# Performance work log

Hardware: AMD Instinct MI355X
Metric: run time of the kernel (lower is better)

The kernel has to match this reference:

```python
import jax, jax.numpy as jnp
import numpy as np

N, E, R, G, IN, H, C = 100000, 400000, 4, 64, 64, 128, 2


def setup_inputs() -> dict:
    key = jax.random.key(0)
    ks = jax.random.split(key, 20)
    s = 0.05
    inp = {
        "x": jax.random.normal(ks[0], (N, IN), jnp.float32),
        "src": jax.random.randint(ks[1], (R, E), 0, N, jnp.int32),
        "dst": jax.random.randint(ks[2], (R, E), 0, N, jnp.int32),
        "graph_ids": jnp.sort(jax.random.randint(ks[3], (N,), 0, G, jnp.int32)),
        "W_in": jax.random.normal(ks[4], (IN, H), jnp.float32) * s,
        "b_in": jnp.zeros((H,), jnp.float32),
        "W1": jax.random.normal(ks[5], (R, H, H), jnp.float32) * s,
        "b1": jnp.zeros((R, H), jnp.float32),
        "W2": jax.random.normal(ks[6], (R, H, H), jnp.float32) * s,
        "b2": jnp.zeros((R, H), jnp.float32),
        "Wm1": jax.random.normal(ks[7], (H, H), jnp.float32) * s,
        "bm1": jnp.zeros((H,), jnp.float32),
        "Wm2": jax.random.normal(ks[8], (H, H), jnp.float32) * s,
        "bm2": jnp.zeros((H,), jnp.float32),
        "Wm3": jax.random.normal(ks[9], (H, C), jnp.float32) * s,
        "bm3": jnp.zeros((C,), jnp.float32),
    }
    return inp


def _gconv(x, src, dst, W, b):
    # DGL GraphConv, norm='both': D_in^{-1/2} A^T D_out^{-1/2} x W + b
    ones_e = jnp.ones(src.shape[0], x.dtype)
    deg_out = jnp.maximum(jax.ops.segment_sum(ones_e, src, num_segments=N), 1.0)
    deg_in = jnp.maximum(jax.ops.segment_sum(ones_e, dst, num_segments=N), 1.0)
    m = x * jax.lax.rsqrt(deg_out)[:, None]          # [N,H] normalized source feats
    agg = jax.ops.segment_sum(m[src], dst, num_segments=N)  # scatter-add over edges
    agg = agg * jax.lax.rsqrt(deg_in)[:, None]
    return agg @ W + b


def _hetero_layer(x, src, dst, W, b):
    # HeteroGraphConv with aggregate='sum' over relations
    out = jnp.zeros((N, W.shape[-1]), x.dtype)
    for r in range(R):
        out = out + _gconv(x, src[r], dst[r], W[r], b[r])
    return out


def reference(x, src, dst, graph_ids, W_in, b_in, W1, b1, W2, b2, Wm1, bm1, Wm2, bm2, Wm3, bm3):
    h = jax.nn.relu(x @ W_in + b_in)                 # input_linear + ReLU
    h = jax.nn.relu(_hetero_layer(h, src, dst, W1, b1))  # RGCN conv1 + ReLU
    h = _hetero_layer(h, src, dst, W2, b2)               # RGCN conv2
    # per-graph mean pooling (replaces the Python element loop)
    counts = jnp.maximum(jax.ops.segment_sum(jnp.ones(N, h.dtype), graph_ids, num_segments=G), 1.0)
    pooled = jax.ops.segment_sum(h, graph_ids, num_segments=G) / counts[:, None]
    # MLP head
    z = jax.nn.relu(pooled @ Wm1 + bm1)
    z = jax.nn.relu(z @ Wm2 + bm2)
    return z @ Wm3 + bm3                             # [G, C]
```

## Files before the change

kernel.cpp:

```cpp
#include <hip/hip_runtime.h>

constexpr int kN = 100000;
constexpr int kE = 400000;
constexpr int kR = 4;
constexpr int kG = 64;
constexpr int kIN = 64;
constexpr int kH = 128;
constexpr int kC = 2;
constexpr int kMAXD = 24;

constexpr size_t SZ_HB16 = (size_t)kN * kH * 2;
constexpr size_t SZ_RN   = (size_t)kR * kN * 4;
constexpr size_t OFF_HA   = 0;
constexpr size_t OFF_HB   = OFF_HA + SZ_HB16;
constexpr size_t OFF_DEGO = OFF_HB + SZ_HB16;
constexpr size_t OFF_CNT  = OFF_DEGO + SZ_RN;
constexpr size_t OFF_RSO  = OFF_CNT + SZ_RN;
constexpr size_t OFF_ELL  = OFF_RSO + SZ_RN;
constexpr size_t OFF_POOL = OFF_ELL + (size_t)kR * kN * kMAXD * 8;
constexpr size_t OFF_Z1   = OFF_POOL + (size_t)kG * kH * 4;
constexpr size_t OFF_Z2   = OFF_Z1 + (size_t)kG * kH * 4;
constexpr size_t OFF_WB1  = OFF_Z2 + (size_t)kG * kH * 4;
constexpr size_t OFF_WB2  = OFF_WB1 + (size_t)kH * kR * kH * 2;

typedef __attribute__((ext_vector_type(8))) short bf16x8;
typedef __attribute__((ext_vector_type(4))) float f32x4;

__device__ inline unsigned short f2bf(float f) {
    unsigned u = __builtin_bit_cast(unsigned, f);
    u += 0x7FFFu + ((u >> 16) & 1u);
    return (unsigned short)(u >> 16);
}
__device__ inline float bf2f_lo(unsigned p) {
    unsigned u = p << 16;
    return __builtin_bit_cast(float, u);
}
__device__ inline float bf2f_hi(unsigned p) {
    unsigned u = p & 0xFFFF0000u;
    return __builtin_bit_cast(float, u);
}


__global__ void k_deg(const int* __restrict__ src, int* __restrict__ deg_o) {
    int i = blockIdx.x * blockDim.x + threadIdx.x;
    if (i >= kR * kE) return;
    int r = i / kE;
    atomicAdd(&deg_o[r * kN + src[i]], 1);
}

__global__ void k_rs(const int* __restrict__ deg, float* __restrict__ rs) {
    int i = blockIdx.x * blockDim.x + threadIdx.x;
    if (i >= kR * kN) return;
    rs[i] = rsqrtf((float)max(deg[i], 1));
}

__global__ void k_fill(const int* __restrict__ src, const int* __restrict__ dst,
                       const float* __restrict__ rs_o, int* __restrict__ cnt,
                       int2* __restrict__ ell) {
    int i = blockIdx.x * blockDim.x + threadIdx.x;
    if (i >= kR * kE) return;
    int r = i / kE;
    int s = src[i], d = dst[i];
    int pos = atomicAdd(&cnt[r * kN + d], 1);
    if (pos < kMAXD) {
        float co = rs_o[r * kN + s];
        ell[(size_t)(r * kN + d) * kMAXD + pos] = make_int2(s, __builtin_bit_cast(int, co));
    }
}

__global__ void k_wconv(const float* __restrict__ W, unsigned short* __restrict__ Wbt) {
    int i = blockIdx.x * 256 + threadIdx.x;
    if (i >= kR * kH * kH) return;
    int r = i >> 14; int kk = (i >> 7) & 127; int j = i & 127;
    Wbt[(size_t)j * (kR * kH) + r * kH + kk] = f2bf(W[i]);
}

__global__ __launch_bounds__(256) void k_inlin(const float* __restrict__ x,
                                               const float* __restrict__ W,
                                               const float* __restrict__ b,
                                               unsigned short* __restrict__ h) {
    __shared__ float Ws[64][128];
    __shared__ float xs[64][64];
    int t = threadIdx.x;
    int n0 = blockIdx.x * 64;
    for (int i = t; i < 64 * 128; i += 256) Ws[i >> 7][i & 127] = W[i];
    for (int i = t; i < 64 * 64; i += 256) {
        int rr = i >> 6, cc = i & 63;
        int n = n0 + rr;
        xs[rr][cc] = (n < kN) ? x[(size_t)n * kIN + cc] : 0.f;
    }
    __syncthreads();
    int jg = t & 31, j0 = jg * 4, rg = t >> 5;
    float acc[8][4] = {};
    for (int k = 0; k < 64; k++) {
        float4 wv = *(const float4*)&Ws[k][j0];
        #pragma unroll
        for (int i = 0; i < 8; i++) {
            float av = xs[rg * 8 + i][k];
            acc[i][0] += av * wv.x; acc[i][1] += av * wv.y;
            acc[i][2] += av * wv.z; acc[i][3] += av * wv.w;
        }
    }
    #pragma unroll
    for (int i = 0; i < 8; i++) {
        int n = n0 + rg * 8 + i;
        if (n < kN) {
            ushort4 res;
            res.x = f2bf(fmaxf(acc[i][0] + b[j0 + 0], 0.f));
            res.y = f2bf(fmaxf(acc[i][1] + b[j0 + 1], 0.f));
            res.z = f2bf(fmaxf(acc[i][2] + b[j0 + 2], 0.f));
            res.w = f2bf(fmaxf(acc[i][3] + b[j0 + 3], 0.f));
            *(ushort4*)&h[(size_t)n * kH + j0] = res;
        }
    }
}

__global__ __launch_bounds__(256, 5) void k_layer(
    const unsigned short* __restrict__ hin, const int2* __restrict__ ell,
    const int* __restrict__ cnt, const unsigned short* __restrict__ Wbt,
    const float* __restrict__ brel, unsigned short* __restrict__ out, int doRelu) {
    __shared__ char Asb[32 * 512 * 2];
    int t = threadIdx.x, wave = t >> 6, lane = t & 63;
    int grp = lane >> 4, li = lane & 15;
    int n0 = blockIdx.x * 32;

    #pragma unroll 1
    for (int batch = 0; batch < 2; batch++) {
        int ni = wave * 8 + batch * 4 + grp;
        int n = n0 + ni;
        #pragma unroll
        for (int r = 0; r < kR; r++) {
            int c = min(cnt[r * kN + n], kMAXD);
            const int2* ep = ell + (size_t)(r * kN + n) * kMAXD;
            float rsi = rsqrtf((float)max(c, 1));
            int cm = c;
            cm = max(cm, __shfl_xor(cm, 16));
            cm = max(cm, __shfl_xor(cm, 32));
            float a0 = 0.f, a1 = 0.f, a2 = 0.f, a3 = 0.f;
            float a4 = 0.f, a5 = 0.f, a6 = 0.f, a7 = 0.f;
            for (int e0 = 0; e0 < cm; e0 += 8) {
                int2 ev[8];
                #pragma unroll
                for (int u = 0; u < 8; u++) ev[u] = ep[min(e0 + u, kMAXD - 1)];
                uint4 pv[8];
                float co[8];
                #pragma unroll
                for (int u = 0; u < 8; u++) {
                    bool k = (e0 + u) < c;
                    int idx = k ? ev[u].x : 0;
                    co[u] = k ? __builtin_bit_cast(float, ev[u].y) : 0.f;
                    pv[u] = *(const uint4*)(hin + (size_t)idx * kH + li * 8);
                }
                #pragma unroll
                for (int u = 0; u < 8; u++) {
                    float cu = co[u];
                    a0 += cu * bf2f_lo(pv[u].x); a1 += cu * bf2f_hi(pv[u].x);
                    a2 += cu * bf2f_lo(pv[u].y); a3 += cu * bf2f_hi(pv[u].y);
                    a4 += cu * bf2f_lo(pv[u].z); a5 += cu * bf2f_hi(pv[u].z);
                    a6 += cu * bf2f_lo(pv[u].w); a7 += cu * bf2f_hi(pv[u].w);
                }
            }
            a0 *= rsi; a1 *= rsi; a2 *= rsi; a3 *= rsi;
            a4 *= rsi; a5 *= rsi; a6 *= rsi; a7 *= rsi;
            uint4 pk;
            pk.x = (unsigned)f2bf(a0) | ((unsigned)f2bf(a1) << 16);
            pk.y = (unsigned)f2bf(a2) | ((unsigned)f2bf(a3) << 16);
            pk.z = (unsigned)f2bf(a4) | ((unsigned)f2bf(a5) << 16);
            pk.w = (unsigned)f2bf(a6) | ((unsigned)f2bf(a7) << 16);
            int byte = ni * 1024 + ((r * 256 + li * 16) ^ ((ni & 7) << 4));
            *(uint4*)(Asb + byte) = pk;
        }
    }
    __syncthreads();

    int colA = lane & 15;
    int kgrp = lane >> 4;
    f32x4 acc00 = {}, acc01 = {}, acc10 = {}, acc11 = {};
    const unsigned short* Wb0 = Wbt + (size_t)(wave * 32 + colA) * 512;
    const unsigned short* Wb1 = Wbt + (size_t)(wave * 32 + 16 + colA) * 512;
    int rowA0 = colA, rowA1 = 16 + colA;
    int abase0 = rowA0 * 1024, abase1 = rowA1 * 1024;
    int asw0 = (rowA0 & 7) << 4, asw1 = (rowA1 & 7) << 4;
    for (int kb = 0; kb < 16; kb++) {
        int kbyte = kb * 64 + kgrp * 16;
        bf16x8 af0 = *(const bf16x8*)(Asb + abase0 + (kbyte ^ asw0));
        bf16x8 af1 = *(const bf16x8*)(Asb + abase1 + (kbyte ^ asw1));
        int koff = kb * 32 + kgrp * 8;
        bf16x8 bf0 = *(const bf16x8*)(Wb0 + koff);
        bf16x8 bf1 = *(const bf16x8*)(Wb1 + koff);
        acc00 = __builtin_amdgcn_mfma_f32_16x16x32_bf16(af0, bf0, acc00, 0, 0, 0);
        acc01 = __builtin_amdgcn_mfma_f32_16x16x32_bf16(af0, bf1, acc01, 0, 0, 0);
        acc10 = __builtin_amdgcn_mfma_f32_16x16x32_bf16(af1, bf0, acc10, 0, 0, 0);
        acc11 = __builtin_amdgcn_mfma_f32_16x16x32_bf16(af1, bf1, acc11, 0, 0, 0);
    }
    int col0 = wave * 32 + colA;
    int col1 = wave * 32 + 16 + colA;
    float bias0 = brel[col0] + brel[128 + col0] + brel[256 + col0] + brel[384 + col0];
    float bias1 = brel[col1] + brel[128 + col1] + brel[256 + col1] + brel[384 + col1];
    #pragma unroll
    for (int j = 0; j < 4; j++) {
        int nA = n0 + kgrp * 4 + j;
        int nB = n0 + 16 + kgrp * 4 + j;
        float v00 = acc00[j] + bias0, v01 = acc01[j] + bias1;
        float v10 = acc10[j] + bias0, v11 = acc11[j] + bias1;
        if (doRelu) {
            v00 = fmaxf(v00, 0.f); v01 = fmaxf(v01, 0.f);
            v10 = fmaxf(v10, 0.f); v11 = fmaxf(v11, 0.f);
        }
        out[(size_t)nA * kH + col0] = f2bf(v00);
        out[(size_t)nA * kH + col1] = f2bf(v01);
        out[(size_t)nB * kH + col0] = f2bf(v10);
        out[(size_t)nB * kH + col1] = f2bf(v11);
    }
}

__global__ void k_pool_acc(const unsigned short* __restrict__ h,
                           const int* __restrict__ gid,
                           float* __restrict__ pooled) {
    int j = threadIdx.x;
    int base = blockIdx.x * 128;
    if (base >= kN) return;
    int end = min(base + 128, kN);
    int curg = gid[base];
    float acc = 0.f;
    for (int n = base; n < end; n++) {
        int g = gid[n];
        if (g != curg) {
            atomicAdd(&pooled[curg * kH + j], acc);
            acc = 0.f; curg = g;
        }
        unsigned short v = h[(size_t)n * kH + j];
        acc += __builtin_bit_cast(float, (unsigned)v << 16);
    }
    atomicAdd(&pooled[curg * kH + j], acc);
}

__global__ void k_head(const float* __restrict__ in, const float* __restrict__ W,
                       const float* __restrict__ b, float* __restrict__ outv,
                       int doRelu, const int* __restrict__ gid) {
    __shared__ float ps[128];
    int g = blockIdx.x, j = threadIdx.x;
    float v = in[g * kH + j];
    if (gid) {
        int lo = 0, hi = kN;
        while (lo < hi) { int m = (lo + hi) >> 1; if (gid[m] < g) lo = m + 1; else hi = m; }
        int s = lo;
        lo = s; hi = kN;
        while (lo < hi) { int m = (lo + hi) >> 1; if (gid[m] <= g) lo = m + 1; else hi = m; }
        v /= (float)max(lo - s, 1);
    }
    ps[j] = v;
    __syncthreads();
    float acc = b[j];
    for (int k = 0; k < kH; k++) acc += ps[k] * W[k * kH + j];
    outv[g * kH + j] = doRelu ? fmaxf(acc, 0.f) : acc;
}

__global__ void k_head3(const float* __restrict__ z, const float* __restrict__ W,
                        const float* __restrict__ b, float* __restrict__ outv) {
    int t = threadIdx.x;
    int g = t >> 1, c = t & 1;
    float acc = b[c];
    for (int k = 0; k < kH; k++) acc += z[g * kH + k] * W[k * kC + c];
    outv[g * kC + c] = acc;
}

extern "C" void kernel_launch(void* const* d_in, const int* in_sizes, int n_in,
                              void* d_out, int out_size, void* d_ws, size_t ws_size,
                              hipStream_t stream) {
    (void)in_sizes; (void)n_in; (void)out_size; (void)ws_size;
    const float* x    = (const float*)d_in[0];
    const int*   src  = (const int*)d_in[1];
    const int*   dst  = (const int*)d_in[2];
    const int*   gid  = (const int*)d_in[3];
    const float* W_in = (const float*)d_in[4];
    const float* b_in = (const float*)d_in[5];
    const float* W1   = (const float*)d_in[6];
    const float* b1   = (const float*)d_in[7];
    const float* W2   = (const float*)d_in[8];
    const float* b2   = (const float*)d_in[9];
    const float* Wm1  = (const float*)d_in[10];
    const float* bm1  = (const float*)d_in[11];
    const float* Wm2  = (const float*)d_in[12];
    const float* bm2  = (const float*)d_in[13];
    const float* Wm3  = (const float*)d_in[14];
    const float* bm3  = (const float*)d_in[15];
    float* out = (float*)d_out;

    char* ws = (char*)d_ws;
    unsigned short* h_a = (unsigned short*)(ws + OFF_HA);
    unsigned short* h_b = (unsigned short*)(ws + OFF_HB);
    int*   deg_o   = (int*)(ws + OFF_DEGO);
    int*   cnt     = (int*)(ws + OFF_CNT);
    float* rs_o    = (float*)(ws + OFF_RSO);
    int2*  ell     = (int2*)(ws + OFF_ELL);
    float* pooled  = (float*)(ws + OFF_POOL);
    float* z1      = (float*)(ws + OFF_Z1);
    float* z2      = (float*)(ws + OFF_Z2);
    unsigned short* wb1 = (unsigned short*)(ws + OFF_WB1);
    unsigned short* wb2 = (unsigned short*)(ws + OFF_WB2);

    hipMemsetAsync(ws + OFF_DEGO, 0, 2 * SZ_RN, stream);
    hipMemsetAsync(ws + OFF_POOL, 0, (size_t)kG * kH * 4, stream);

    int egrid = (kR * kE + 255) / 256;
    k_deg<<<egrid, 256, 0, stream>>>(src, deg_o);
    k_rs<<<(kR * kN + 255) / 256, 256, 0, stream>>>(deg_o, rs_o);
    k_fill<<<egrid, 256, 0, stream>>>(src, dst, rs_o, cnt, ell);

    k_wconv<<<(kR * kH * kH + 255) / 256, 256, 0, stream>>>(W1, wb1);
    k_wconv<<<(kR * kH * kH + 255) / 256, 256, 0, stream>>>(W2, wb2);

    k_inlin<<<(kN + 63) / 64, 256, 0, stream>>>(x, W_in, b_in, h_a);

    k_layer<<<kN / 32, 256, 0, stream>>>(h_a, ell, cnt, wb1, b1, h_b, 1);
    k_layer<<<kN / 32, 256, 0, stream>>>(h_b, ell, cnt, wb2, b2, h_a, 0);

    k_pool_acc<<<(kN + 127) / 128, 128, 0, stream>>>(h_a, gid, pooled);
    k_head<<<kG, 128, 0, stream>>>(pooled, Wm1, bm1, z1, 1, gid);
    k_head<<<kG, 128, 0, stream>>>(z1, Wm2, bm2, z2, 1, nullptr);
    k_head3<<<1, 128, 0, stream>>>(z2, Wm3, bm3, out);
}
```

Measured before the change: 579.3 us.

## Halve layer block tile to 16 nodes, fuse rsqrt into fill, merge weight conversions

Each layer block now handles 16 nodes instead of 32, with one gather batch and half the LDS. Launch bounds move from 5 to 8 blocks per CU so more waves can hide gather latency. The separate rsqrt kernel is removed and the degree normalization is computed inside the ELL fill. The two weight-conversion launches are merged into one. The trade-off is that each weight fragment loaded from global memory is reused across only one A row tile instead of two, which doubles weight reads per node.

```diff
diff --git a/kernel.cpp b/kernel.cpp
--- a/kernel.cpp
+++ b/kernel.cpp
@@ -15,8 +15,7 @@
 constexpr size_t OFF_HB   = OFF_HA + SZ_HB16;
 constexpr size_t OFF_DEGO = OFF_HB + SZ_HB16;
 constexpr size_t OFF_CNT  = OFF_DEGO + SZ_RN;
-constexpr size_t OFF_RSO  = OFF_CNT + SZ_RN;
-constexpr size_t OFF_ELL  = OFF_RSO + SZ_RN;
+constexpr size_t OFF_ELL  = OFF_CNT + SZ_RN;
 constexpr size_t OFF_POOL = OFF_ELL + (size_t)kR * kN * kMAXD * 8;
 constexpr size_t OFF_Z1   = OFF_POOL + (size_t)kG * kH * 4;
 constexpr size_t OFF_Z2   = OFF_Z1 + (size_t)kG * kH * 4;
@@ -48,14 +47,8 @@
     atomicAdd(&deg_o[r * kN + src[i]], 1);
 }
 
-__global__ void k_rs(const int* __restrict__ deg, float* __restrict__ rs) {
-    int i = blockIdx.x * blockDim.x + threadIdx.x;
-    if (i >= kR * kN) return;
-    rs[i] = rsqrtf((float)max(deg[i], 1));
-}
-
 __global__ void k_fill(const int* __restrict__ src, const int* __restrict__ dst,
-                       const float* __restrict__ rs_o, int* __restrict__ cnt,
+                       const int* __restrict__ deg_o, int* __restrict__ cnt,
                        int2* __restrict__ ell) {
     int i = blockIdx.x * blockDim.x + threadIdx.x;
     if (i >= kR * kE) return;
@@ -63,16 +56,20 @@
     int s = src[i], d = dst[i];
     int pos = atomicAdd(&cnt[r * kN + d], 1);
     if (pos < kMAXD) {
-        float co = rs_o[r * kN + s];
+        float co = rsqrtf((float)max(deg_o[r * kN + s], 1));
         ell[(size_t)(r * kN + d) * kMAXD + pos] = make_int2(s, __builtin_bit_cast(int, co));
     }
 }
 
-__global__ void k_wconv(const float* __restrict__ W, unsigned short* __restrict__ Wbt) {
+__global__ void k_wconv(const float* __restrict__ W1, const float* __restrict__ W2,
+                        unsigned short* __restrict__ Wbt1, unsigned short* __restrict__ Wbt2) {
     int i = blockIdx.x * 256 + threadIdx.x;
-    if (i >= kR * kH * kH) return;
-    int r = i >> 14; int kk = (i >> 7) & 127; int j = i & 127;
-    Wbt[(size_t)j * (kR * kH) + r * kH + kk] = f2bf(W[i]);
+    if (i >= 2 * kR * kH * kH) return;
+    const float* W = (i < kR * kH * kH) ? W1 : W2;
+    unsigned short* Wbt = (i < kR * kH * kH) ? Wbt1 : Wbt2;
+    int ii = i & (kR * kH * kH - 1);
+    int r = ii >> 14; int kk = (ii >> 7) & 127; int j = ii & 127;
+    Wbt[(size_t)j * (kR * kH) + r * kH + kk] = f2bf(W[ii]);
 }
 
 __global__ __launch_bounds__(256) void k_inlin(const float* __restrict__ x,
@@ -115,18 +112,17 @@
     }
 }
 
-__global__ __launch_bounds__(256, 5) void k_layer(
+__global__ __launch_bounds__(256, 8) void k_layer(
     const unsigned short* __restrict__ hin, const int2* __restrict__ ell,
     const int* __restrict__ cnt, const unsigned short* __restrict__ Wbt,
     const float* __restrict__ brel, unsigned short* __restrict__ out, int doRelu) {
-    __shared__ char Asb[32 * 512 * 2];
+    __shared__ char Asb[16 * 1024];
     int t = threadIdx.x, wave = t >> 6, lane = t & 63;
     int grp = lane >> 4, li = lane & 15;
-    int n0 = blockIdx.x * 32;
-
-    #pragma unroll 1
-    for (int batch = 0; batch < 2; batch++) {
-        int ni = wave * 8 + batch * 4 + grp;
+    int n0 = blockIdx.x * 16;
+
+    {
+        int ni = wave * 4 + grp;
         int n = n0 + ni;
         #pragma unroll
         for (int r = 0; r < kR; r++) {
@@ -175,23 +171,20 @@
 
     int colA = lane & 15;
     int kgrp = lane >> 4;
-    f32x4 acc00 = {}, acc01 = {}, acc10 = {}, acc11 = {};
+    f32x4 acc0 = {}, acc1 = {};
     const unsigned short* Wb0 = Wbt + (size_t)(wave * 32 + colA) * 512;
     const unsigned short* Wb1 = Wbt + (size_t)(wave * 32 + 16 + colA) * 512;
-    int rowA0 = colA, rowA1 = 16 + colA;
-    int abase0 = rowA0 * 1024, abase1 = rowA1 * 1024;
-    int asw0 = (rowA0 & 7) << 4, asw1 = (rowA1 & 7) << 4;
+    int rowA = colA;
+    int abase = rowA * 1024;
+    int asw = (rowA & 7) << 4;
     for (int kb = 0; kb < 16; kb++) {
         int kbyte = kb * 64 + kgrp * 16;
-        bf16x8 af0 = *(const bf16x8*)(Asb + abase0 + (kbyte ^ asw0));
-        bf16x8 af1 = *(const bf16x8*)(Asb + abase1 + (kbyte ^ asw1));
+        bf16x8 af = *(const bf16x8*)(Asb + abase + (kbyte ^ asw));
         int koff = kb * 32 + kgrp * 8;
         bf16x8 bf0 = *(const bf16x8*)(Wb0 + koff);
         bf16x8 bf1 = *(const bf16x8*)(Wb1 + koff);
-        acc00 = __builtin_amdgcn_mfma_f32_16x16x32_bf16(af0, bf0, acc00, 0, 0, 0);
-        acc01 = __builtin_amdgcn_mfma_f32_16x16x32_bf16(af0, bf1, acc01, 0, 0, 0);
-        acc10 = __builtin_amdgcn_mfma_f32_16x16x32_bf16(af1, bf0, acc10, 0, 0, 0);
-        acc11 = __builtin_amdgcn_mfma_f32_16x16x32_bf16(af1, bf1, acc11, 0, 0, 0);
+        acc0 = __builtin_amdgcn_mfma_f32_16x16x32_bf16(af, bf0, acc0, 0, 0, 0);
+        acc1 = __builtin_amdgcn_mfma_f32_16x16x32_bf16(af, bf1, acc1, 0, 0, 0);
     }
     int col0 = wave * 32 + colA;
     int col1 = wave * 32 + 16 + colA;
@@ -199,18 +192,11 @@
     float bias1 = brel[col1] + brel[128 + col1] + brel[256 + col1] + brel[384 + col1];
     #pragma unroll
     for (int j = 0; j < 4; j++) {
-        int nA = n0 + kgrp * 4 + j;
-        int nB = n0 + 16 + kgrp * 4 + j;
-        float v00 = acc00[j] + bias0, v01 = acc01[j] + bias1;
-        float v10 = acc10[j] + bias0, v11 = acc11[j] + bias1;
-        if (doRelu) {
-            v00 = fmaxf(v00, 0.f); v01 = fmaxf(v01, 0.f);
-            v10 = fmaxf(v10, 0.f); v11 = fmaxf(v11, 0.f);
-        }
-        out[(size_t)nA * kH + col0] = f2bf(v00);
-        out[(size_t)nA * kH + col1] = f2bf(v01);
-        out[(size_t)nB * kH + col0] = f2bf(v10);
-        out[(size_t)nB * kH + col1] = f2bf(v11);
+        int n = n0 + kgrp * 4 + j;
+        float v0 = acc0[j] + bias0, v1 = acc1[j] + bias1;
+        if (doRelu) { v0 = fmaxf(v0, 0.f); v1 = fmaxf(v1, 0.f); }
+        out[(size_t)n * kH + col0] = f2bf(v0);
+        out[(size_t)n * kH + col1] = f2bf(v1);
     }
 }
 
@@ -292,7 +278,6 @@
     unsigned short* h_b = (unsigned short*)(ws + OFF_HB);
     int*   deg_o   = (int*)(ws + OFF_DEGO);
     int*   cnt     = (int*)(ws + OFF_CNT);
-    float* rs_o    = (float*)(ws + OFF_RSO);
     int2*  ell     = (int2*)(ws + OFF_ELL);
     float* pooled  = (float*)(ws + OFF_POOL);
     float* z1      = (float*)(ws + OFF_Z1);
@@ -305,16 +290,14 @@
 
     int egrid = (kR * kE + 255) / 256;
     k_deg<<<egrid, 256, 0, stream>>>(src, deg_o);
-    k_rs<<<(kR * kN + 255) / 256, 256, 0, stream>>>(deg_o, rs_o);
-    k_fill<<<egrid, 256, 0, stream>>>(src, dst, rs_o, cnt, ell);
-
-    k_wconv<<<(kR * kH * kH + 255) / 256, 256, 0, stream>>>(W1, wb1);
-    k_wconv<<<(kR * kH * kH + 255) / 256, 256, 0, stream>>>(W2, wb2);
+    k_fill<<<egrid, 256, 0, stream>>>(src, dst, deg_o, cnt, ell);
+
+    k_wconv<<<(2 * kR * kH * kH + 255) / 256, 256, 0, stream>>>(W1, W2, wb1, wb2);
 
     k_inlin<<<(kN + 63) / 64, 256, 0, stream>>>(x, W_in, b_in, h_a);
 
-    k_layer<<<kN / 32, 256, 0, stream>>>(h_a, ell, cnt, wb1, b1, h_b, 1);
-    k_layer<<<kN / 32, 256, 0, stream>>>(h_b, ell, cnt, wb2, b2, h_a, 0);
+    k_layer<<<kN / 16, 256, 0, stream>>>(h_a, ell, cnt, wb1, b1, h_b, 1);
+    k_layer<<<kN / 16, 256, 0, stream>>>(h_b, ell, cnt, wb2, b2, h_a, 0);
 
     k_pool_acc<<<(kN + 127) / 128, 128, 0, stream>>>(h_a, gid, pooled);
     k_head<<<kG, 128, 0, stream>>>(pooled, Wm1, bm1, z1, 1, gid);
```

After: 742.3 us. +28.1%, slower.

## Fuse graph preprocessing into one build kernel and compute source norms on the fly

Applied to the files above, without the earlier changes.

Merges the out-degree count, rsqrt and ELL fill kernels into one edge pass. The ELL now stores only source indices (4 bytes instead of 8), and the layer kernel computes the per-edge coefficient from the out-degree array at gather time. The two weight-conversion launches are merged into one. This removes two preprocessing passes and halves ELL storage and traffic, at the cost of an extra dependent gather of deg_o plus an rsqrt per edge inside the layer loop.

```diff
diff --git a/kernel.cpp b/kernel.cpp
--- a/kernel.cpp
+++ b/kernel.cpp
@@ -15,9 +15,8 @@
 constexpr size_t OFF_HB   = OFF_HA + SZ_HB16;
 constexpr size_t OFF_DEGO = OFF_HB + SZ_HB16;
 constexpr size_t OFF_CNT  = OFF_DEGO + SZ_RN;
-constexpr size_t OFF_RSO  = OFF_CNT + SZ_RN;
-constexpr size_t OFF_ELL  = OFF_RSO + SZ_RN;
-constexpr size_t OFF_POOL = OFF_ELL + (size_t)kR * kN * kMAXD * 8;
+constexpr size_t OFF_ELL  = OFF_CNT + SZ_RN;
+constexpr size_t OFF_POOL = OFF_ELL + (size_t)kR * kN * kMAXD * 4;
 constexpr size_t OFF_Z1   = OFF_POOL + (size_t)kG * kH * 4;
 constexpr size_t OFF_Z2   = OFF_Z1 + (size_t)kG * kH * 4;
 constexpr size_t OFF_WB1  = OFF_Z2 + (size_t)kG * kH * 4;
@@ -40,39 +39,29 @@
     return __builtin_bit_cast(float, u);
 }
 
-
-__global__ void k_deg(const int* __restrict__ src, int* __restrict__ deg_o) {
-    int i = blockIdx.x * blockDim.x + threadIdx.x;
-    if (i >= kR * kE) return;
-    int r = i / kE;
-    atomicAdd(&deg_o[r * kN + src[i]], 1);
-}
-
-__global__ void k_rs(const int* __restrict__ deg, float* __restrict__ rs) {
-    int i = blockIdx.x * blockDim.x + threadIdx.x;
-    if (i >= kR * kN) return;
-    rs[i] = rsqrtf((float)max(deg[i], 1));
-}
-
-__global__ void k_fill(const int* __restrict__ src, const int* __restrict__ dst,
-                       const float* __restrict__ rs_o, int* __restrict__ cnt,
-                       int2* __restrict__ ell) {
+__global__ void k_build(const int* __restrict__ src, const int* __restrict__ dst,
+                        int* __restrict__ deg_o, int* __restrict__ cnt,
+                        int* __restrict__ ell) {
     int i = blockIdx.x * blockDim.x + threadIdx.x;
     if (i >= kR * kE) return;
     int r = i / kE;
     int s = src[i], d = dst[i];
+    atomicAdd(&deg_o[r * kN + s], 1);
     int pos = atomicAdd(&cnt[r * kN + d], 1);
     if (pos < kMAXD) {
-        float co = rs_o[r * kN + s];
-        ell[(size_t)(r * kN + d) * kMAXD + pos] = make_int2(s, __builtin_bit_cast(int, co));
-    }
-}
-
-__global__ void k_wconv(const float* __restrict__ W, unsigned short* __restrict__ Wbt) {
+        ell[(size_t)(r * kN + d) * kMAXD + pos] = s;
+    }
+}
+
+__global__ void k_wconv(const float* __restrict__ W1, const float* __restrict__ W2,
+                        unsigned short* __restrict__ Wbt1, unsigned short* __restrict__ Wbt2) {
     int i = blockIdx.x * 256 + threadIdx.x;
-    if (i >= kR * kH * kH) return;
-    int r = i >> 14; int kk = (i >> 7) & 127; int j = i & 127;
-    Wbt[(size_t)j * (kR * kH) + r * kH + kk] = f2bf(W[i]);
+    if (i >= 2 * kR * kH * kH) return;
+    const float* W = (i < kR * kH * kH) ? W1 : W2;
+    unsigned short* Wbt = (i < kR * kH * kH) ? Wbt1 : Wbt2;
+    int ii = i & (kR * kH * kH - 1);
+    int r = ii >> 14; int kk = (ii >> 7) & 127; int j = ii & 127;
+    Wbt[(size_t)j * (kR * kH) + r * kH + kk] = f2bf(W[ii]);
 }
 
 __global__ __launch_bounds__(256) void k_inlin(const float* __restrict__ x,
@@ -116,9 +105,10 @@
 }
 
 __global__ __launch_bounds__(256, 5) void k_layer(
-    const unsigned short* __restrict__ hin, const int2* __restrict__ ell,
-    const int* __restrict__ cnt, const unsigned short* __restrict__ Wbt,
-    const float* __restrict__ brel, unsigned short* __restrict__ out, int doRelu) {
+    const unsigned short* __restrict__ hin, const int* __restrict__ ell,
+    const int* __restrict__ cnt, const int* __restrict__ dego,
+    const unsigned short* __restrict__ Wbt, const float* __restrict__ brel,
+    unsigned short* __restrict__ out, int doRelu) {
     __shared__ char Asb[32 * 512 * 2];
     int t = threadIdx.x, wave = t >> 6, lane = t & 63;
     int grp = lane >> 4, li = lane & 15;
@@ -131,7 +121,8 @@
         #pragma unroll
         for (int r = 0; r < kR; r++) {
             int c = min(cnt[r * kN + n], kMAXD);
-            const int2* ep = ell + (size_t)(r * kN + n) * kMAXD;
+            const int* ep = ell + (size_t)(r * kN + n) * kMAXD;
+            const int* dgo = dego + r * kN;
             float rsi = rsqrtf((float)max(c, 1));
             int cm = c;
             cm = max(cm, __shfl_xor(cm, 16));
@@ -139,7 +130,7 @@
             float a0 = 0.f, a1 = 0.f, a2 = 0.f, a3 = 0.f;
             float a4 = 0.f, a5 = 0.f, a6 = 0.f, a7 = 0.f;
             for (int e0 = 0; e0 < cm; e0 += 8) {
-                int2 ev[8];
+                int ev[8];
                 #pragma unroll
                 for (int u = 0; u < 8; u++) ev[u] = ep[min(e0 + u, kMAXD - 1)];
                 uint4 pv[8];
@@ -147,8 +138,8 @@
                 #pragma unroll
                 for (int u = 0; u < 8; u++) {
                     bool k = (e0 + u) < c;
-                    int idx = k ? ev[u].x : 0;
-                    co[u] = k ? __builtin_bit_cast(float, ev[u].y) : 0.f;
+                    int idx = k ? ev[u] : 0;
+                    co[u] = k ? rsqrtf((float)max(dgo[idx], 1)) : 0.f;
                     pv[u] = *(const uint4*)(hin + (size_t)idx * kH + li * 8);
                 }
                 #pragma unroll
@@ -292,8 +283,7 @@
     unsigned short* h_b = (unsigned short*)(ws + OFF_HB);
     int*   deg_o   = (int*)(ws + OFF_DEGO);
     int*   cnt     = (int*)(ws + OFF_CNT);
-    float* rs_o    = (float*)(ws + OFF_RSO);
-    int2*  ell     = (int2*)(ws + OFF_ELL);
+    int*   ell     = (int*)(ws + OFF_ELL);
     float* pooled  = (float*)(ws + OFF_POOL);
     float* z1      = (float*)(ws + OFF_Z1);
     float* z2      = (float*)(ws + OFF_Z2);
@@ -304,17 +294,14 @@
     hipMemsetAsync(ws + OFF_POOL, 0, (size_t)kG * kH * 4, stream);
 
     int egrid = (kR * kE + 255) / 256;
-    k_deg<<<egrid, 256, 0, stream>>>(src, deg_o);
-    k_rs<<<(kR * kN + 255) / 256, 256, 0, stream>>>(deg_o, rs_o);
-    k_fill<<<egrid, 256, 0, stream>>>(src, dst, rs_o, cnt, ell);
-
-    k_wconv<<<(kR * kH * kH + 255) / 256, 256, 0, stream>>>(W1, wb1);
-    k_wconv<<<(kR * kH * kH + 255) / 256, 256, 0, stream>>>(W2, wb2);
+    k_build<<<egrid, 256, 0, stream>>>(src, dst, deg_o, cnt, ell);
+
+    k_wconv<<<(2 * kR * kH * kH + 255) / 256, 256, 0, stream>>>(W1, W2, wb1, wb2);
 
     k_inlin<<<(kN + 63) / 64, 256, 0, stream>>>(x, W_in, b_in, h_a);
 
-    k_layer<<<kN / 32, 256, 0, stream>>>(h_a, ell, cnt, wb1, b1, h_b, 1);
-    k_layer<<<kN / 32, 256, 0, stream>>>(h_b, ell, cnt, wb2, b2, h_a, 0);
+    k_layer<<<kN / 32, 256, 0, stream>>>(h_a, ell, cnt, deg_o, wb1, b1, h_b, 1);
+    k_layer<<<kN / 32, 256, 0, stream>>>(h_b, ell, cnt, deg_o, wb2, b2, h_a, 0);
 
     k_pool_acc<<<(kN + 127) / 128, 128, 0, stream>>>(h_a, gid, pooled);
     k_head<<<kG, 128, 0, stream>>>(pooled, Wm1, bm1, z1, 1, gid);
```

Result: slower. 675.3 us (+16.6%).
